# Kernel tuning notes

Hardware: AMD Instinct MI355X
Metric: run time of the kernel (lower is better)

The kernel has to match this reference:

```python
import jax, jax.numpy as jnp
import numpy as np

N = 50000
E = 800000
G = 8  # number of graphs
D_IN, D_H, D_OUT = 300, 128, 64


def _linear_params(key, d_out, d_in):
    k1, k2 = jax.random.split(key)
    s = 1.0 / np.sqrt(d_in)
    W = jax.random.uniform(k1, (d_out, d_in), minval=-s, maxval=s, dtype=jnp.float32)
    b = jax.random.uniform(k2, (d_out,), minval=-s, maxval=s, dtype=jnp.float32)
    return W, b


def setup_inputs() -> dict:
    key = jax.random.key(0)
    ks = jax.random.split(key, 10)
    x = jax.random.normal(ks[0], (N, D_IN), dtype=jnp.float32)
    edge_index = jax.random.randint(ks[1], (2, E), 0, N, dtype=jnp.int64)
    batch = jnp.sort(jax.random.randint(ks[2], (N,), 0, G, dtype=jnp.int64))
    W_emb, b_emb = _linear_params(ks[3], D_H, D_IN)
    # SAGEConv layer 0: lin_l (neighbors, with bias), lin_r (root, no bias)
    Wl0, bl0 = _linear_params(ks[4], D_H, D_H)
    Wr0, _ = _linear_params(ks[5], D_H, D_H)
    # SAGEConv layer 1
    Wl1, bl1 = _linear_params(ks[6], D_H, D_H)
    Wr1, _ = _linear_params(ks[7], D_H, D_H)
    W_att, b_att = _linear_params(ks[8], 1, D_H)
    W_out, b_out = _linear_params(ks[9], D_OUT, D_H)
    return {
        "x": x, "edge_index": edge_index, "batch": batch,
        "W_emb": W_emb, "b_emb": b_emb,
        "Wl0": Wl0, "bl0": bl0, "Wr0": Wr0,
        "Wl1": Wl1, "bl1": bl1, "Wr1": Wr1,
        "W_att": W_att, "b_att": b_att,
        "W_out": W_out, "b_out": b_out,
    }


def _sage_conv(h, src, dst, Wl, bl, Wr):
    # mean aggregation of source-node features onto destination nodes
    agg = jax.ops.segment_sum(h[src], dst, num_segments=N)  # [N, D_H]
    deg = jax.ops.segment_sum(jnp.ones((src.shape[0],), dtype=h.dtype), dst, num_segments=N)
    agg = agg / jnp.maximum(deg, 1.0)[:, None]
    return agg @ Wl.T + bl + h @ Wr.T


def reference(x, edge_index, batch, W_emb, b_emb, Wl0, bl0, Wr0, Wl1, bl1, Wr1,
              W_att, b_att, W_out, b_out):
    src, dst = edge_index[0], edge_index[1]
    h = x @ W_emb.T + b_emb                       # [N, D_H]
    h = jax.nn.relu(_sage_conv(h, src, dst, Wl0, bl0, Wr0))
    h = jax.nn.relu(_sage_conv(h, src, dst, Wl1, bl1, Wr1))
    # attention readout: softmax over ALL nodes (dim=0), as in original code
    scores = h @ W_att.T + b_att                  # [N, 1]
    weights = jax.nn.softmax(scores, axis=0)      # [N, 1]
    pooled = jax.ops.segment_sum(h * weights, batch, num_segments=G)  # [G, D_H]
    return pooled @ W_out.T + b_out               # [G, D_OUT]
```

## Files before the change

kernel.cpp:

```cpp
#include <hip/hip_runtime.h>
#include <math.h>

#define D_H 128

typedef __attribute__((ext_vector_type(8))) __bf16 bf16x8;
typedef __attribute__((ext_vector_type(4))) float f32x4;

__device__ __forceinline__ void split_bf16(float v, unsigned short& hi, unsigned short& lo) {
  unsigned int u = __float_as_uint(v);
  hi = (unsigned short)(u >> 16);
  float l = v - __uint_as_float(u & 0xffff0000u);
  lo = (unsigned short)(__float_as_uint(l) >> 16);
}

__device__ __forceinline__ float blo(unsigned int u) { return __uint_as_float(u << 16); }
__device__ __forceinline__ float bhi(unsigned int u) { return __uint_as_float(u & 0xffff0000u); }

__device__ __forceinline__ void pack_pair8(const float* xv, bf16x8& ah, bf16x8& al) {
  union { bf16x8 v; unsigned int u[4]; } H, L;
#pragma unroll
  for (int e = 0; e < 4; ++e) {
    unsigned int u0 = __float_as_uint(xv[2 * e]);
    unsigned int u1 = __float_as_uint(xv[2 * e + 1]);
    float l0 = xv[2 * e] - __uint_as_float(u0 & 0xffff0000u);
    float l1 = xv[2 * e + 1] - __uint_as_float(u1 & 0xffff0000u);
    H.u[e] = (u0 >> 16) | (u1 & 0xffff0000u);
    L.u[e] = (__float_as_uint(l0) >> 16) | (__float_as_uint(l1) & 0xffff0000u);
  }
  ah = H.v;
  al = L.v;
}

__device__ __forceinline__ void load_lds16(const void* g, void* l) {
  __builtin_amdgcn_global_load_lds((const __attribute__((address_space(1))) unsigned int*)g,
                                   (__attribute__((address_space(3))) unsigned int*)l,
                                   16, 0, 0);
}


__global__ __launch_bounds__(256) void k_hist(const int* __restrict__ dstv,
                                              int* __restrict__ bucketCnt, int E) {
  __shared__ int h[256];
  int t = threadIdx.x;
  h[t] = 0;
  __syncthreads();
  for (int i = blockIdx.x * 256 + t; i < E; i += gridDim.x * 256)
    atomicAdd(&h[dstv[i] >> 8], 1);
  __syncthreads();
  if (h[t]) atomicAdd(&bucketCnt[t], h[t]);
}

__global__ __launch_bounds__(256) void k_bucketscan(const int* __restrict__ bucketCnt, int NB,
                                                    int* __restrict__ bucketBase,
                                                    int* __restrict__ cursor,
                                                    int* __restrict__ row_ptr, int N, int E) {
  __shared__ int s[256];
  int t = threadIdx.x;
  int v = (t < NB) ? bucketCnt[t] : 0;
  s[t] = v;
  __syncthreads();
  for (int off = 1; off < 256; off <<= 1) {
    int u = (t >= off) ? s[t - off] : 0;
    __syncthreads();
    s[t] += u;
    __syncthreads();
  }
  int excl = s[t] - v;
  if (t < NB) {
    bucketBase[t] = excl;
    cursor[t] = excl;
  }
  if (t == NB - 1) bucketBase[NB] = excl + v;
  if (t == 0) row_ptr[N] = E;
}

__global__ __launch_bounds__(256) void k_binscatter(const int* __restrict__ srcv,
                                                    const int* __restrict__ dstv,
                                                    int* __restrict__ cursor,
                                                    unsigned int* __restrict__ tmp, int E) {
  __shared__ int h[256];
  __shared__ int base[256];
  int t = threadIdx.x;
  int chunk = (E + gridDim.x - 1) / gridDim.x;
  int c0 = blockIdx.x * chunk;
  int c1 = min(c0 + chunk, E);
  int dst[16], src[16];
  h[t] = 0;
  __syncthreads();
#pragma unroll
  for (int p = 0; p < 16; ++p) {
    int i = c0 + p * 256 + t;
    if (i < c1) {
      dst[p] = dstv[i];
      src[p] = srcv[i];
      atomicAdd(&h[dst[p] >> 8], 1);
    } else {
      dst[p] = -1;
      src[p] = 0;
    }
  }
  __syncthreads();
  int cnt = h[t];
  __syncthreads();
  base[t] = cnt ? atomicAdd(&cursor[t], cnt) : 0;
  h[t] = 0;
  __syncthreads();
#pragma unroll
  for (int p = 0; p < 16; ++p) {
    if (dst[p] >= 0) {
      int b = dst[p] >> 8;
      int pos = base[b] + atomicAdd(&h[b], 1);
      tmp[pos] = (unsigned int)src[p] | ((unsigned int)(dst[p] & 255) << 16);
    }
  }
}

__global__ __launch_bounds__(256) void k_localcsr(const unsigned int* __restrict__ tmp,
                                                  const int* __restrict__ bucketBase,
                                                  int* __restrict__ row_ptr,
                                                  int* __restrict__ col, int N) {
  __shared__ int deg[256], rp[256], cur[256];
  int b = blockIdx.x, t = threadIdx.x;
  int s = bucketBase[b], e = bucketBase[b + 1];
  int epb = e - s;
  deg[t] = 0;
  __syncthreads();
  for (int i = t; i < epb; i += 256) atomicAdd(&deg[tmp[s + i] >> 16], 1);
  __syncthreads();
  int v = deg[t];
  rp[t] = v;
  __syncthreads();
  for (int off = 1; off < 256; off <<= 1) {
    int u = (t >= off) ? rp[t - off] : 0;
    __syncthreads();
    rp[t] += u;
    __syncthreads();
  }
  int excl = rp[t] - v;
  rp[t] = excl;
  cur[t] = 0;
  int gid = b * 256 + t;
  if (gid < N) row_ptr[gid] = s + excl;
  __syncthreads();
  for (int i = t; i < epb; i += 256) {
    unsigned int p = tmp[s + i];
    int dl = p >> 16;
    int pos = s + rp[dl] + atomicAdd(&cur[dl], 1);
    col[pos] = (int)(p & 0xffffu);
  }
}


__global__ __launch_bounds__(256) void k_wsplit(
    const float* __restrict__ Wemb, const float* __restrict__ Wl0,
    const float* __restrict__ Wr0, const float* __restrict__ Wl1,
    const float* __restrict__ Wr1, unsigned short* __restrict__ WembP,
    unsigned short* __restrict__ P0l, unsigned short* __restrict__ P0r,
    unsigned short* __restrict__ P1l, unsigned short* __restrict__ P1r) {
  int tid = blockIdx.x * 256 + threadIdx.x;
  const int EMB = 128 * 320;
  if (tid < EMB) {
    int o = tid / 320, k = tid - o * 320;
    float v = (k < 300) ? Wemb[o * 300 + k] : 0.f;
    unsigned short h, l;
    split_bf16(v, h, l);
    int sw = ((2 * k) ^ ((o & 7) << 4)) >> 1;
    WembP[o * 640 + sw] = h;
    WembP[o * 640 + 320 + sw] = l;
  } else if (tid < EMB + 4 * 16384) {
    int r = tid - EMB;
    int m = r >> 14;
    int i = r & 16383;
    int o = i >> 7, k = i & 127;
    const float* W = (m == 0) ? Wl0 : (m == 1) ? Wr0 : (m == 2) ? Wl1 : Wr1;
    unsigned short* P = (m == 0) ? P0l : (m == 1) ? P0r : (m == 2) ? P1l : P1r;
    unsigned short h, l;
    split_bf16(W[o * 128 + k], h, l);
    int sw = ((2 * k) ^ ((o & 7) << 4)) >> 1;
    P[o * 256 + sw] = h;
    P[o * 256 + 128 + sw] = l;
  }
}


__global__ __launch_bounds__(512, 4) void k_emb(const float* __restrict__ x,
                                                const unsigned short* __restrict__ Wp,
                                                const float* __restrict__ bias,
                                                unsigned short* __restrict__ P, int N) {
  __shared__ alignas(16) char sW[49152];
  int t = threadIdx.x, lane = t & 63, wave = t >> 6;
  int ch = blockIdx.y;
  int row0 = blockIdx.x * 128;
  int fr = lane & 15, q4 = lane >> 4;
  int X = (fr & 7) << 4;
  int row = row0 + wave * 16 + fr;
  if (row >= N) row = N - 1;
  const float* xrp = x + (size_t)row * 300;
  const char* Wbase = (const char*)Wp + (size_t)ch * 64 * 1280;
  f32x4 acc[4] = {};
  float xb[2][8];

  auto stage = [&](int CB, int HS, int kb, int nround) {
    for (int r = 0; r < nround; ++r) {
      int off = r * 8192 + wave * 1024;
      int offl = off + lane * 16;
      int c = offl / CB;
      int w = offl - c * CB;
      const char* src = Wbase + (size_t)c * 1280 + (w < HS ? kb + w : 640 + kb + (w - HS));
      load_lds16(src, sW + off);
    }
  };
  auto loadx = [&](float* d, int c0) {
    if (c0 + 7 < 300) {
      float4 a = *(const float4*)(xrp + c0);
      float4 b = *(const float4*)(xrp + c0 + 4);
      d[0] = a.x; d[1] = a.y; d[2] = a.z; d[3] = a.w;
      d[4] = b.x; d[5] = b.y; d[6] = b.z; d[7] = b.w;
    } else {
#pragma unroll
      for (int e = 0; e < 8; ++e) d[e] = (c0 + e < 300) ? xrp[c0 + e] : 0.f;
    }
  };

  stage(768, 384, 0, 6);
  loadx(xb[0], q4 * 8);
  __syncthreads();

#pragma unroll
  for (int ks = 0; ks < 6; ++ks) {
    loadx(xb[(ks + 1) & 1], (ks + 1) * 32 + q4 * 8);
    bf16x8 bh[4], bl[4];
#pragma unroll
    for (int j = 0; j < 4; ++j) {
      int c64 = j * 16 + fr;
      int ko = (ks * 64 + q4 * 16) ^ X;
      bh[j] = *(const bf16x8*)(sW + c64 * 768 + ko);
      bl[j] = *(const bf16x8*)(sW + c64 * 768 + 384 + ko);
    }
    bf16x8 ah, al;
    pack_pair8(xb[ks & 1], ah, al);
#pragma unroll
    for (int j = 0; j < 4; ++j) {
      acc[j] = __builtin_amdgcn_mfma_f32_16x16x32_bf16(ah, bh[j], acc[j], 0, 0, 0);
      acc[j] = __builtin_amdgcn_mfma_f32_16x16x32_bf16(ah, bl[j], acc[j], 0, 0, 0);
      acc[j] = __builtin_amdgcn_mfma_f32_16x16x32_bf16(al, bh[j], acc[j], 0, 0, 0);
    }
  }
  __syncthreads();
  stage(512, 256, 384, 4);
  __syncthreads();

#pragma unroll
  for (int ks2 = 0; ks2 < 4; ++ks2) {
    int ks = 6 + ks2;
    if (ks < 9) loadx(xb[(ks + 1) & 1], (ks + 1) * 32 + q4 * 8);
    bf16x8 bh[4], bl[4];
#pragma unroll
    for (int j = 0; j < 4; ++j) {
      int c64 = j * 16 + fr;
      int ko = (ks2 * 64 + q4 * 16) ^ X;
      bh[j] = *(const bf16x8*)(sW + c64 * 512 + ko);
      bl[j] = *(const bf16x8*)(sW + c64 * 512 + 256 + ko);
    }
    bf16x8 ah, al;
    pack_pair8(xb[ks & 1], ah, al);
#pragma unroll
    for (int j = 0; j < 4; ++j) {
      acc[j] = __builtin_amdgcn_mfma_f32_16x16x32_bf16(ah, bh[j], acc[j], 0, 0, 0);
      acc[j] = __builtin_amdgcn_mfma_f32_16x16x32_bf16(ah, bl[j], acc[j], 0, 0, 0);
      acc[j] = __builtin_amdgcn_mfma_f32_16x16x32_bf16(al, bh[j], acc[j], 0, 0, 0);
    }
  }
  __syncthreads();

  float* T = (float*)sW;
#pragma unroll
  for (int j = 0; j < 4; ++j) {
    float b = bias[ch * 64 + j * 16 + fr];
#pragma unroll
    for (int rg = 0; rg < 4; ++rg)
      T[(wave * 16 + q4 * 4 + rg) * 66 + j * 16 + fr] = acc[j][rg] + b;
  }
  __syncthreads();
  int rr = t >> 2, q = t & 3;
  float vals[16];
#pragma unroll
  for (int c = 0; c < 16; ++c) vals[c] = T[rr * 66 + q * 16 + c];
  unsigned int hu[8], lu[8];
#pragma unroll
  for (int e = 0; e < 8; ++e) {
    unsigned int u0 = __float_as_uint(vals[2 * e]);
    unsigned int u1 = __float_as_uint(vals[2 * e + 1]);
    float l0 = vals[2 * e] - __uint_as_float(u0 & 0xffff0000u);
    float l1 = vals[2 * e + 1] - __uint_as_float(u1 & 0xffff0000u);
    hu[e] = (u0 >> 16) | (u1 & 0xffff0000u);
    lu[e] = (__float_as_uint(l0) >> 16) | (__float_as_uint(l1) & 0xffff0000u);
  }
  char* rowp = (char*)P + (size_t)(row0 + rr) * 512 + ch * 128;
  *(uint4*)(rowp + q * 32) = make_uint4(hu[0], hu[1], hu[2], hu[3]);
  *(uint4*)(rowp + q * 32 + 16) = make_uint4(hu[4], hu[5], hu[6], hu[7]);
  *(uint4*)(rowp + 256 + q * 32) = make_uint4(lu[0], lu[1], lu[2], lu[3]);
  *(uint4*)(rowp + 256 + q * 32 + 16) = make_uint4(lu[4], lu[5], lu[6], lu[7]);
}


__global__ __launch_bounds__(512, 4) void k_conv(const unsigned short* __restrict__ Ap,
                                                 const unsigned short* __restrict__ Wl,
                                                 const unsigned short* __restrict__ Wr,
                                                 unsigned short* __restrict__ Ub,
                                                 float* __restrict__ V) {
  __shared__ alignas(16) char sW[65536];
  int t = threadIdx.x, lane = t & 63, wave = t >> 6;
  int wr = wave >> 1, wc = wave & 1;
  int om = blockIdx.y;
  const char* Wg = (const char*)(om ? Wr : Wl);
  int row0 = blockIdx.x * 128;
  int fr = lane & 15, q4 = lane >> 4;
  int X = (fr & 7) << 4;

  for (int r = 0; r < 8; ++r) {
    int off = r * 8192 + wave * 1024;
    load_lds16(Wg + off + lane * 16, sW + off);
  }

  const char* a0 = (const char*)Ap + (size_t)(row0 + wr * 32 + fr) * 512 + q4 * 16;
  const char* a1 = a0 + 16 * 512;
  bf16x8 ah[2][2], al[2][2];
  ah[0][0] = *(const bf16x8*)a0;
  al[0][0] = *(const bf16x8*)(a0 + 256);
  ah[0][1] = *(const bf16x8*)a1;
  al[0][1] = *(const bf16x8*)(a1 + 256);

  f32x4 acc[2][4] = {};
  __syncthreads();

#pragma unroll
  for (int ks = 0; ks < 4; ++ks) {
    if (ks < 3) {
      int nb = (ks + 1) * 64;
      ah[(ks + 1) & 1][0] = *(const bf16x8*)(a0 + nb);
      al[(ks + 1) & 1][0] = *(const bf16x8*)(a0 + nb + 256);
      ah[(ks + 1) & 1][1] = *(const bf16x8*)(a1 + nb);
      al[(ks + 1) & 1][1] = *(const bf16x8*)(a1 + nb + 256);
    }
#pragma unroll
    for (int j = 0; j < 4; ++j) {
      int c = wc * 64 + j * 16 + fr;
      int ko = (ks * 64 + q4 * 16) ^ X;
      bf16x8 bh = *(const bf16x8*)(sW + c * 512 + ko);
      bf16x8 bl = *(const bf16x8*)(sW + c * 512 + 256 + ko);
#pragma unroll
      for (int i = 0; i < 2; ++i) {
        acc[i][j] = __builtin_amdgcn_mfma_f32_16x16x32_bf16(ah[ks & 1][i], bh, acc[i][j], 0, 0, 0);
        acc[i][j] = __builtin_amdgcn_mfma_f32_16x16x32_bf16(ah[ks & 1][i], bl, acc[i][j], 0, 0, 0);
        acc[i][j] = __builtin_amdgcn_mfma_f32_16x16x32_bf16(al[ks & 1][i], bh, acc[i][j], 0, 0, 0);
      }
    }
  }

  if (om == 0) {
    __syncthreads();
    unsigned short* Tb = (unsigned short*)sW;
#pragma unroll
    for (int i = 0; i < 2; ++i)
#pragma unroll
      for (int j = 0; j < 4; ++j)
#pragma unroll
        for (int rg = 0; rg < 4; ++rg) {
          float v = acc[i][j][rg];
          unsigned int u = __float_as_uint(v);
          u += 0x7fffu + ((u >> 16) & 1);
          Tb[(wr * 32 + i * 16 + q4 * 4 + rg) * 132 + wc * 64 + j * 16 + fr] =
              (unsigned short)(u >> 16);
        }
    __syncthreads();
    int rr = t >> 2, q = t & 3;
    const unsigned short* src = Tb + rr * 132 + q * 32;
    uint4 o0 = *(const uint4*)src;
    uint4 o1 = *(const uint4*)(src + 8);
    uint4 o2 = *(const uint4*)(src + 16);
    uint4 o3 = *(const uint4*)(src + 24);
    char* drow = (char*)Ub + (size_t)(row0 + rr) * 256 + q * 64;
    *(uint4*)(drow) = o0;
    *(uint4*)(drow + 16) = o1;
    *(uint4*)(drow + 32) = o2;
    *(uint4*)(drow + 48) = o3;
  } else {
#pragma unroll
    for (int i = 0; i < 2; ++i)
#pragma unroll
      for (int j = 0; j < 4; ++j)
#pragma unroll
        for (int rg = 0; rg < 4; ++rg)
          V[(size_t)(row0 + wr * 32 + i * 16 + q4 * 4 + rg) * D_H + wc * 64 + j * 16 + fr] =
              acc[i][j][rg];
  }
}


template <int OUTP>
__global__ __launch_bounds__(256) void k_aggfin(const unsigned short* __restrict__ Ub,
                                                float* __restrict__ V,
                                                const float* __restrict__ bias,
                                                const int* __restrict__ row_ptr,
                                                const int* __restrict__ col,
                                                unsigned short* __restrict__ Hp,
                                                const float* __restrict__ watt,
                                                const float* __restrict__ batt,
                                                float* __restrict__ scores,
                                                float* __restrict__ partmax, int N) {
  __shared__ float smax[4];
  int wv = threadIdx.x >> 6;
  int wid = blockIdx.x * 4 + wv;
  int lane = threadIdx.x & 63;
  bool valid = wid < N;
  if (OUTP == 1 && !valid) return;

  int half = lane >> 5;
  int dq = lane & 31;
  float a0 = 0.f, a1 = 0.f, a2 = 0.f, a3 = 0.f;
  float o0 = 0.f, o1 = 0.f, o2 = 0.f, o3 = 0.f;

  if (valid) {
    const uint2* uvb = (const uint2*)Ub;
    int e0 = row_ptr[wid], e1 = row_ptr[wid + 1];
    int e = e0;
    for (; e + 8 <= e1; e += 8) {
      int s0 = col[e + half];
      int s1 = col[e + 2 + half];
      int s2 = col[e + 4 + half];
      int s3 = col[e + 6 + half];
      uint2 u0 = uvb[(size_t)s0 * 32 + dq];
      uint2 u1 = uvb[(size_t)s1 * 32 + dq];
      uint2 u2 = uvb[(size_t)s2 * 32 + dq];
      uint2 u3 = uvb[(size_t)s3 * 32 + dq];
      a0 += blo(u0.x) + blo(u1.x) + blo(u2.x) + blo(u3.x);
      a1 += bhi(u0.x) + bhi(u1.x) + bhi(u2.x) + bhi(u3.x);
      a2 += blo(u0.y) + blo(u1.y) + blo(u2.y) + blo(u3.y);
      a3 += bhi(u0.y) + bhi(u1.y) + bhi(u2.y) + bhi(u3.y);
    }
    for (; e + 2 <= e1; e += 2) {
      uint2 u = uvb[(size_t)col[e + half] * 32 + dq];
      a0 += blo(u.x);
      a1 += bhi(u.x);
      a2 += blo(u.y);
      a3 += bhi(u.y);
    }
    if (e < e1 && half == 0) {
      uint2 u = uvb[(size_t)col[e] * 32 + dq];
      a0 += blo(u.x);
      a1 += bhi(u.x);
      a2 += blo(u.y);
      a3 += bhi(u.y);
    }
    a0 += __shfl_xor(a0, 32);
    a1 += __shfl_xor(a1, 32);
    a2 += __shfl_xor(a2, 32);
    a3 += __shfl_xor(a3, 32);

    float inv = 1.f / fmaxf((float)(e1 - e0), 1.f);
    float4 vv = *(const float4*)(V + (size_t)wid * D_H + dq * 4);
    float4 bb = *(const float4*)(bias + dq * 4);
    o0 = fmaxf(a0 * inv + vv.x + bb.x, 0.f);
    o1 = fmaxf(a1 * inv + vv.y + bb.y, 0.f);
    o2 = fmaxf(a2 * inv + vv.z + bb.z, 0.f);
    o3 = fmaxf(a3 * inv + vv.w + bb.w, 0.f);

    if (OUTP) {
      unsigned int w0, w1;
      if (half == 0) {
        unsigned int x0 = __float_as_uint(o0), x1 = __float_as_uint(o1);
        unsigned int x2 = __float_as_uint(o2), x3 = __float_as_uint(o3);
        w0 = (x0 >> 16) | (x1 & 0xffff0000u);
        w1 = (x2 >> 16) | (x3 & 0xffff0000u);
      } else {
        unsigned short h, lq0, lq1, lq2, lq3;
        split_bf16(o0, h, lq0);
        split_bf16(o1, h, lq1);
        split_bf16(o2, h, lq2);
        split_bf16(o3, h, lq3);
        w0 = (unsigned int)lq0 | ((unsigned int)lq1 << 16);
        w1 = (unsigned int)lq2 | ((unsigned int)lq3 << 16);
      }
      *(uint2*)((char*)Hp + (size_t)wid * 512 + half * 256 + dq * 8) = make_uint2(w0, w1);
    } else {
      if (half == 0)
        *(float4*)(V + (size_t)wid * D_H + dq * 4) = make_float4(o0, o1, o2, o3);
    }
  }

  if (OUTP == 0) {
    float sc = -3.0e38f;
    float4 w = valid ? *(const float4*)(watt + dq * 4) : make_float4(0.f, 0.f, 0.f, 0.f);
    float p = o0 * w.x + o1 * w.y + o2 * w.z + o3 * w.w;
#pragma unroll
    for (int off = 1; off < 32; off <<= 1) p += __shfl_xor(p, off);
    if (valid) {
      sc = p + batt[0];
      if (lane == 0) scores[wid] = sc;
    }
    if (lane == 0) smax[wv] = sc;
    __syncthreads();
    if (threadIdx.x == 0)
      partmax[blockIdx.x] = fmaxf(fmaxf(smax[0], smax[1]), fmaxf(smax[2], smax[3]));
  }
}


__global__ __launch_bounds__(256) void k_redmax(const float* __restrict__ partmax, int PB,
                                                float* __restrict__ red) {
  __shared__ float sm[256];
  int t = threadIdx.x;
  float m = -3.0e38f;
  for (int i = t; i < PB; i += 256) m = fmaxf(m, partmax[i]);
  sm[t] = m;
  __syncthreads();
  for (int off = 128; off > 0; off >>= 1) {
    if (t < off) sm[t] = fmaxf(sm[t], sm[t + off]);
    __syncthreads();
  }
  if (t == 0) {
    red[0] = sm[0];
    red[1] = 0.f;
  }
  for (int i = t; i < 1024; i += 256) red[2 + i] = 0.f;
}

__global__ __launch_bounds__(256) void k_pool(const float* __restrict__ h,
                                              const float* __restrict__ scores,
                                              const int* __restrict__ batch,
                                              float* __restrict__ red, int N, int nblocks) {
  __shared__ float pl[4][1024];
  __shared__ float zp[4];
  int t = threadIdx.x;
  int w = t >> 6, lane = t & 63;
  for (int i = lane; i < 1024; i += 64) pl[w][i] = 0.f;
  float M = red[0];
  float zacc = 0.f;
  const float2* hv = (const float2*)h;
  int stride = nblocks * 4;
  for (int node = blockIdx.x * 4 + w; node < N; node += stride) {
    float wgt = __expf(scores[node] - M);
    int b = batch[node];
    float2 v = hv[(size_t)node * 64 + lane];
    pl[w][b * 128 + lane * 2] += v.x * wgt;
    pl[w][b * 128 + lane * 2 + 1] += v.y * wgt;
    zacc += wgt;
  }
  if (lane == 0) zp[w] = zacc;
  __syncthreads();
  for (int i = t; i < 1024; i += 256) {
    float s = pl[0][i] + pl[1][i] + pl[2][i] + pl[3][i];
    atomicAdd(&red[2 + i], s);
  }
  if (t == 0) atomicAdd(&red[1], zp[0] + zp[1] + zp[2] + zp[3]);
}

__global__ __launch_bounds__(512) void k_out(const float* __restrict__ red,
                                             const float* __restrict__ Wout,
                                             const float* __restrict__ bout,
                                             float* __restrict__ out) {
  int t = threadIdx.x;
  int gIdx = t >> 6, o = t & 63;
  float invZ = 1.f / red[1];
  const float* p = red + 2 + gIdx * 128;
  const float* wr = Wout + (size_t)o * 128;
  float acc = 0.f;
  for (int k = 0; k < 128; ++k) acc = fmaf(p[k], wr[k], acc);
  out[gIdx * 64 + o] = acc * invZ + bout[o];
}


extern "C" void kernel_launch(void* const* d_in, const int* in_sizes, int n_in,
                              void* d_out, int out_size, void* d_ws, size_t ws_size,
                              hipStream_t stream) {
  const float* x     = (const float*)d_in[0];
  const int*   ei    = (const int*)d_in[1];
  const int*   batch = (const int*)d_in[2];
  const float* W_emb = (const float*)d_in[3];
  const float* b_emb = (const float*)d_in[4];
  const float* Wl0   = (const float*)d_in[5];
  const float* bl0   = (const float*)d_in[6];
  const float* Wr0   = (const float*)d_in[7];
  const float* Wl1   = (const float*)d_in[8];
  const float* bl1   = (const float*)d_in[9];
  const float* Wr1   = (const float*)d_in[10];
  const float* W_att = (const float*)d_in[11];
  const float* b_att = (const float*)d_in[12];
  const float* W_out = (const float*)d_in[13];
  const float* b_out = (const float*)d_in[14];
  float* out = (float*)d_out;

  const int DIN = 300;
  int N = in_sizes[0] / DIN;
  int E = in_sizes[1] / 2;
  int Npad = (N + 127) & ~127;
  int NB = (N + 255) / 256;

  char* wsp = (char*)d_ws;
  size_t off = 0;
  auto carve = [&](size_t bytes) -> void* {
    void* p = wsp + off;
    off += (bytes + 255) & ~(size_t)255;
    return p;
  };
  unsigned short* P  = (unsigned short*)carve((size_t)Npad * 512);
  unsigned short* Ub = (unsigned short*)carve((size_t)Npad * 256);
  float*          V  = (float*)carve((size_t)Npad * 512);
  unsigned short* WembP = (unsigned short*)carve((size_t)128 * 640 * 2);
  unsigned short* WP0l  = (unsigned short*)carve((size_t)128 * 256 * 2);
  unsigned short* WP0r  = (unsigned short*)carve((size_t)128 * 256 * 2);
  unsigned short* WP1l  = (unsigned short*)carve((size_t)128 * 256 * 2);
  unsigned short* WP1r  = (unsigned short*)carve((size_t)128 * 256 * 2);
  int*   colA    = (int*)carve((size_t)E * 4);
  unsigned int* tmpE = (unsigned int*)carve((size_t)E * 4);
  int*   row_ptr = (int*)carve((size_t)(N + 1) * 4);
  int*   bucketCnt  = (int*)carve((size_t)(NB + 1) * 4);
  int*   bucketBase = (int*)carve((size_t)(NB + 1) * 4);
  int*   cursor     = (int*)carve((size_t)(NB + 1) * 4);
  float* scores  = (float*)carve((size_t)N * 4);
  int aggBlocks = (N + 3) / 4;
  float* partmax = (float*)carve((size_t)aggBlocks * 4);
  float* red     = (float*)carve((size_t)(2 + 1024) * 4);

  const int* srcv = ei;
  const int* dstv = ei + E;

  hipMemsetAsync(bucketCnt, 0, (size_t)NB * 4, stream);
  k_hist<<<512, 256, 0, stream>>>(dstv, bucketCnt, E);
  k_bucketscan<<<1, 256, 0, stream>>>(bucketCnt, NB, bucketBase, cursor, row_ptr, N, E);
  k_binscatter<<<256, 256, 0, stream>>>(srcv, dstv, cursor, tmpE, E);
  k_localcsr<<<NB, 256, 0, stream>>>(tmpE, bucketBase, row_ptr, colA, N);
  k_wsplit<<<(128 * 320 + 4 * 16384 + 255) / 256, 256, 0, stream>>>(
      W_emb, Wl0, Wr0, Wl1, Wr1, WembP, WP0l, WP0r, WP1l, WP1r);

  dim3 gemb(Npad / 128, 2);
  k_emb<<<gemb, 512, 0, stream>>>(x, WembP, b_emb, P, N);

  dim3 gconv(Npad / 128, 2);
  k_conv<<<gconv, 512, 0, stream>>>(P, WP0l, WP0r, Ub, V);
  k_aggfin<1><<<aggBlocks, 256, 0, stream>>>(Ub, V, bl0, row_ptr, colA, P,
                                             nullptr, nullptr, nullptr, nullptr, N);
  k_conv<<<gconv, 512, 0, stream>>>(P, WP1l, WP1r, Ub, V);
  k_aggfin<0><<<aggBlocks, 256, 0, stream>>>(Ub, V, bl1, row_ptr, colA, nullptr,
                                             W_att, b_att, scores, partmax, N);

  const float* h2 = (const float*)V;
  k_redmax<<<1, 256, 0, stream>>>(partmax, aggBlocks, red);
  k_pool<<<256, 256, 0, stream>>>(h2, scores, batch, red, N, 256);
  k_out<<<1, 512, 0, stream>>>(red, W_out, b_out, out);
}
```

Before: 251.9 us.

## Fuse weight split into histogram, merge pool kernels, restructure emb/conv GEMM tiling

Weight bf16 splitting moves into the histogram kernel, and the redmax, pool and output kernels become one kernel that finishes with a last-block-done counter. Several launches disappear. The embedding and conv GEMMs now cover all 128 output columns per block (one grid dimension instead of two) and stage weights in smaller K-chunks with reduced LDS, so x/A rows are read once rather than twice. This costs more syncs per K-chunk, and every pool block recomputes the global max.

```diff
diff --git a/kernel.cpp b/kernel.cpp
--- a/kernel.cpp
+++ b/kernel.cpp
@@ -38,14 +38,44 @@
 }
 
 
-__global__ __launch_bounds__(256) void k_hist(const int* __restrict__ dstv,
-                                              int* __restrict__ bucketCnt, int E) {
+__global__ __launch_bounds__(256) void k_histw(
+    const int* __restrict__ dstv, int* __restrict__ bucketCnt, int E,
+    const float* __restrict__ Wemb, const float* __restrict__ Wl0,
+    const float* __restrict__ Wr0, const float* __restrict__ Wl1,
+    const float* __restrict__ Wr1, unsigned short* __restrict__ WembP,
+    unsigned short* __restrict__ P0l, unsigned short* __restrict__ P0r,
+    unsigned short* __restrict__ P1l, unsigned short* __restrict__ P1r) {
   __shared__ int h[256];
   int t = threadIdx.x;
   h[t] = 0;
   __syncthreads();
   for (int i = blockIdx.x * 256 + t; i < E; i += gridDim.x * 256)
     atomicAdd(&h[dstv[i] >> 8], 1);
+
+  int tid = blockIdx.x * 256 + t;
+  const int EMB = 128 * 320;
+  if (tid < EMB) {
+    int o = tid / 320, k = tid - o * 320;
+    float v = (k < 300) ? Wemb[o * 300 + k] : 0.f;
+    unsigned short hh, ll;
+    split_bf16(v, hh, ll);
+    int sw = ((2 * k) ^ ((o & 7) << 4)) >> 1;
+    WembP[o * 640 + sw] = hh;
+    WembP[o * 640 + 320 + sw] = ll;
+  } else if (tid < EMB + 4 * 16384) {
+    int r = tid - EMB;
+    int m = r >> 14;
+    int i = r & 16383;
+    int o = i >> 7, k = i & 127;
+    const float* W = (m == 0) ? Wl0 : (m == 1) ? Wr0 : (m == 2) ? Wl1 : Wr1;
+    unsigned short* P = (m == 0) ? P0l : (m == 1) ? P0r : (m == 2) ? P1l : P1r;
+    unsigned short hh, ll;
+    split_bf16(W[o * 128 + k], hh, ll);
+    int sw = ((2 * k) ^ ((o & 7) << 4)) >> 1;
+    P[o * 256 + sw] = hh;
+    P[o * 256 + 128 + sw] = ll;
+  }
+
   __syncthreads();
   if (h[t]) atomicAdd(&bucketCnt[t], h[t]);
 }
@@ -151,65 +181,21 @@
 }
 
 
-__global__ __launch_bounds__(256) void k_wsplit(
-    const float* __restrict__ Wemb, const float* __restrict__ Wl0,
-    const float* __restrict__ Wr0, const float* __restrict__ Wl1,
-    const float* __restrict__ Wr1, unsigned short* __restrict__ WembP,
-    unsigned short* __restrict__ P0l, unsigned short* __restrict__ P0r,
-    unsigned short* __restrict__ P1l, unsigned short* __restrict__ P1r) {
-  int tid = blockIdx.x * 256 + threadIdx.x;
-  const int EMB = 128 * 320;
-  if (tid < EMB) {
-    int o = tid / 320, k = tid - o * 320;
-    float v = (k < 300) ? Wemb[o * 300 + k] : 0.f;
-    unsigned short h, l;
-    split_bf16(v, h, l);
-    int sw = ((2 * k) ^ ((o & 7) << 4)) >> 1;
-    WembP[o * 640 + sw] = h;
-    WembP[o * 640 + 320 + sw] = l;
-  } else if (tid < EMB + 4 * 16384) {
-    int r = tid - EMB;
-    int m = r >> 14;
-    int i = r & 16383;
-    int o = i >> 7, k = i & 127;
-    const float* W = (m == 0) ? Wl0 : (m == 1) ? Wr0 : (m == 2) ? Wl1 : Wr1;
-    unsigned short* P = (m == 0) ? P0l : (m == 1) ? P0r : (m == 2) ? P1l : P1r;
-    unsigned short h, l;
-    split_bf16(W[o * 128 + k], h, l);
-    int sw = ((2 * k) ^ ((o & 7) << 4)) >> 1;
-    P[o * 256 + sw] = h;
-    P[o * 256 + 128 + sw] = l;
-  }
-}
-
-
 __global__ __launch_bounds__(512, 4) void k_emb(const float* __restrict__ x,
                                                 const unsigned short* __restrict__ Wp,
                                                 const float* __restrict__ bias,
                                                 unsigned short* __restrict__ P, int N) {
-  __shared__ alignas(16) char sW[49152];
+  __shared__ alignas(16) char sW[34048];
   int t = threadIdx.x, lane = t & 63, wave = t >> 6;
-  int ch = blockIdx.y;
   int row0 = blockIdx.x * 128;
   int fr = lane & 15, q4 = lane >> 4;
   int X = (fr & 7) << 4;
   int row = row0 + wave * 16 + fr;
   if (row >= N) row = N - 1;
   const float* xrp = x + (size_t)row * 300;
-  const char* Wbase = (const char*)Wp + (size_t)ch * 64 * 1280;
-  f32x4 acc[4] = {};
+  f32x4 acc[8] = {};
   float xb[2][8];
 
-  auto stage = [&](int CB, int HS, int kb, int nround) {
-    for (int r = 0; r < nround; ++r) {
-      int off = r * 8192 + wave * 1024;
-      int offl = off + lane * 16;
-      int c = offl / CB;
-      int w = offl - c * CB;
-      const char* src = Wbase + (size_t)c * 1280 + (w < HS ? kb + w : 640 + kb + (w - HS));
-      load_lds16(src, sW + off);
-    }
-  };
   auto loadx = [&](float* d, int c0) {
     if (c0 + 7 < 300) {
       float4 a = *(const float4*)(xrp + c0);
@@ -222,85 +208,75 @@
     }
   };
 
-  stage(768, 384, 0, 6);
   loadx(xb[0], q4 * 8);
-  __syncthreads();
-
-#pragma unroll
-  for (int ks = 0; ks < 6; ++ks) {
-    loadx(xb[(ks + 1) & 1], (ks + 1) * 32 + q4 * 8);
-    bf16x8 bh[4], bl[4];
-#pragma unroll
-    for (int j = 0; j < 4; ++j) {
-      int c64 = j * 16 + fr;
-      int ko = (ks * 64 + q4 * 16) ^ X;
-      bh[j] = *(const bf16x8*)(sW + c64 * 768 + ko);
-      bl[j] = *(const bf16x8*)(sW + c64 * 768 + 384 + ko);
-    }
-    bf16x8 ah, al;
-    pack_pair8(xb[ks & 1], ah, al);
-#pragma unroll
-    for (int j = 0; j < 4; ++j) {
-      acc[j] = __builtin_amdgcn_mfma_f32_16x16x32_bf16(ah, bh[j], acc[j], 0, 0, 0);
-      acc[j] = __builtin_amdgcn_mfma_f32_16x16x32_bf16(ah, bl[j], acc[j], 0, 0, 0);
-      acc[j] = __builtin_amdgcn_mfma_f32_16x16x32_bf16(al, bh[j], acc[j], 0, 0, 0);
-    }
-  }
-  __syncthreads();
-  stage(512, 256, 384, 4);
-  __syncthreads();
-
-#pragma unroll
-  for (int ks2 = 0; ks2 < 4; ++ks2) {
-    int ks = 6 + ks2;
-    if (ks < 9) loadx(xb[(ks + 1) & 1], (ks + 1) * 32 + q4 * 8);
-    bf16x8 bh[4], bl[4];
-#pragma unroll
-    for (int j = 0; j < 4; ++j) {
-      int c64 = j * 16 + fr;
-      int ko = (ks2 * 64 + q4 * 16) ^ X;
-      bh[j] = *(const bf16x8*)(sW + c64 * 512 + ko);
-      bl[j] = *(const bf16x8*)(sW + c64 * 512 + 256 + ko);
-    }
-    bf16x8 ah, al;
-    pack_pair8(xb[ks & 1], ah, al);
-#pragma unroll
-    for (int j = 0; j < 4; ++j) {
-      acc[j] = __builtin_amdgcn_mfma_f32_16x16x32_bf16(ah, bh[j], acc[j], 0, 0, 0);
-      acc[j] = __builtin_amdgcn_mfma_f32_16x16x32_bf16(ah, bl[j], acc[j], 0, 0, 0);
-      acc[j] = __builtin_amdgcn_mfma_f32_16x16x32_bf16(al, bh[j], acc[j], 0, 0, 0);
-    }
-  }
-  __syncthreads();
+#pragma unroll
+  for (int kc = 0; kc < 5; ++kc) {
+#pragma unroll
+    for (int r = 0; r < 4; ++r) {
+      int off = r * 8192 + wave * 1024;
+      int offl = off + lane * 16;
+      int c = offl >> 8;
+      int w = offl & 255;
+      const char* src = (const char*)Wp + (size_t)c * 1280 +
+                        (w < 128 ? kc * 128 + w : 640 + kc * 128 + (w - 128));
+      load_lds16(src, sW + off);
+    }
+    __syncthreads();
+#pragma unroll
+    for (int s = 0; s < 2; ++s) {
+      int ks = kc * 2 + s;
+      if (ks < 9) loadx(xb[(ks + 1) & 1], (ks + 1) * 32 + q4 * 8);
+      bf16x8 ah, al;
+      pack_pair8(xb[ks & 1], ah, al);
+      int ko = (s * 64 + q4 * 16) ^ X;
+#pragma unroll
+      for (int j = 0; j < 8; ++j) {
+        int c = j * 16 + fr;
+        bf16x8 bh = *(const bf16x8*)(sW + c * 256 + ko);
+        bf16x8 bl = *(const bf16x8*)(sW + c * 256 + 128 + ko);
+        acc[j] = __builtin_amdgcn_mfma_f32_16x16x32_bf16(ah, bh, acc[j], 0, 0, 0);
+        acc[j] = __builtin_amdgcn_mfma_f32_16x16x32_bf16(ah, bl, acc[j], 0, 0, 0);
+        acc[j] = __builtin_amdgcn_mfma_f32_16x16x32_bf16(al, bh, acc[j], 0, 0, 0);
+      }
+    }
+    __syncthreads();
+  }
 
   float* T = (float*)sW;
 #pragma unroll
-  for (int j = 0; j < 4; ++j) {
-    float b = bias[ch * 64 + j * 16 + fr];
-#pragma unroll
-    for (int rg = 0; rg < 4; ++rg)
-      T[(wave * 16 + q4 * 4 + rg) * 66 + j * 16 + fr] = acc[j][rg] + b;
-  }
-  __syncthreads();
-  int rr = t >> 2, q = t & 3;
-  float vals[16];
-#pragma unroll
-  for (int c = 0; c < 16; ++c) vals[c] = T[rr * 66 + q * 16 + c];
-  unsigned int hu[8], lu[8];
-#pragma unroll
-  for (int e = 0; e < 8; ++e) {
-    unsigned int u0 = __float_as_uint(vals[2 * e]);
-    unsigned int u1 = __float_as_uint(vals[2 * e + 1]);
-    float l0 = vals[2 * e] - __uint_as_float(u0 & 0xffff0000u);
-    float l1 = vals[2 * e + 1] - __uint_as_float(u1 & 0xffff0000u);
-    hu[e] = (u0 >> 16) | (u1 & 0xffff0000u);
-    lu[e] = (__float_as_uint(l0) >> 16) | (__float_as_uint(l1) & 0xffff0000u);
-  }
-  char* rowp = (char*)P + (size_t)(row0 + rr) * 512 + ch * 128;
-  *(uint4*)(rowp + q * 32) = make_uint4(hu[0], hu[1], hu[2], hu[3]);
-  *(uint4*)(rowp + q * 32 + 16) = make_uint4(hu[4], hu[5], hu[6], hu[7]);
-  *(uint4*)(rowp + 256 + q * 32) = make_uint4(lu[0], lu[1], lu[2], lu[3]);
-  *(uint4*)(rowp + 256 + q * 32 + 16) = make_uint4(lu[4], lu[5], lu[6], lu[7]);
+  for (int ph = 0; ph < 2; ++ph) {
+    if ((wave >> 2) == ph) {
+      int wl = wave & 3;
+#pragma unroll
+      for (int j = 0; j < 8; ++j) {
+        float b = bias[j * 16 + fr];
+#pragma unroll
+        for (int rg = 0; rg < 4; ++rg)
+          T[(wl * 16 + q4 * 4 + rg) * 132 + j * 16 + fr] = acc[j][rg] + b;
+      }
+    }
+    __syncthreads();
+    int r = t >> 3, q = t & 7;
+    float vals[16];
+#pragma unroll
+    for (int c = 0; c < 16; ++c) vals[c] = T[r * 132 + q * 16 + c];
+    unsigned int hu[8], lu[8];
+#pragma unroll
+    for (int e = 0; e < 8; ++e) {
+      unsigned int u0 = __float_as_uint(vals[2 * e]);
+      unsigned int u1 = __float_as_uint(vals[2 * e + 1]);
+      float l0 = vals[2 * e] - __uint_as_float(u0 & 0xffff0000u);
+      float l1 = vals[2 * e + 1] - __uint_as_float(u1 & 0xffff0000u);
+      hu[e] = (u0 >> 16) | (u1 & 0xffff0000u);
+      lu[e] = (__float_as_uint(l0) >> 16) | (__float_as_uint(l1) & 0xffff0000u);
+    }
+    char* rowp = (char*)P + (size_t)(row0 + ph * 64 + r) * 512;
+    *(uint4*)(rowp + q * 32) = make_uint4(hu[0], hu[1], hu[2], hu[3]);
+    *(uint4*)(rowp + q * 32 + 16) = make_uint4(hu[4], hu[5], hu[6], hu[7]);
+    *(uint4*)(rowp + 256 + q * 32) = make_uint4(lu[0], lu[1], lu[2], lu[3]);
+    *(uint4*)(rowp + 256 + q * 32 + 16) = make_uint4(lu[4], lu[5], lu[6], lu[7]);
+    __syncthreads();
+  }
 }
 
 
@@ -309,92 +285,101 @@
                                                  const unsigned short* __restrict__ Wr,
                                                  unsigned short* __restrict__ Ub,
                                                  float* __restrict__ V) {
-  __shared__ alignas(16) char sW[65536];
+  __shared__ alignas(16) char sW[34048];
   int t = threadIdx.x, lane = t & 63, wave = t >> 6;
-  int wr = wave >> 1, wc = wave & 1;
-  int om = blockIdx.y;
-  const char* Wg = (const char*)(om ? Wr : Wl);
+  int wr2 = wave >> 1, wc = wave & 1;
   int row0 = blockIdx.x * 128;
   int fr = lane & 15, q4 = lane >> 4;
   int X = (fr & 7) << 4;
 
-  for (int r = 0; r < 8; ++r) {
-    int off = r * 8192 + wave * 1024;
-    load_lds16(Wg + off + lane * 16, sW + off);
-  }
-
-  const char* a0 = (const char*)Ap + (size_t)(row0 + wr * 32 + fr) * 512 + q4 * 16;
-  const char* a1 = a0 + 16 * 512;
-  bf16x8 ah[2][2], al[2][2];
-  ah[0][0] = *(const bf16x8*)a0;
-  al[0][0] = *(const bf16x8*)(a0 + 256);
-  ah[0][1] = *(const bf16x8*)a1;
-  al[0][1] = *(const bf16x8*)(a1 + 256);
-
-  f32x4 acc[2][4] = {};
-  __syncthreads();
-
-#pragma unroll
-  for (int ks = 0; ks < 4; ++ks) {
-    if (ks < 3) {
-      int nb = (ks + 1) * 64;
-      ah[(ks + 1) & 1][0] = *(const bf16x8*)(a0 + nb);
-      al[(ks + 1) & 1][0] = *(const bf16x8*)(a0 + nb + 256);
-      ah[(ks + 1) & 1][1] = *(const bf16x8*)(a1 + nb);
-      al[(ks + 1) & 1][1] = *(const bf16x8*)(a1 + nb + 256);
-    }
-#pragma unroll
-    for (int j = 0; j < 4; ++j) {
-      int c = wc * 64 + j * 16 + fr;
-      int ko = (ks * 64 + q4 * 16) ^ X;
-      bf16x8 bh = *(const bf16x8*)(sW + c * 512 + ko);
-      bf16x8 bl = *(const bf16x8*)(sW + c * 512 + 256 + ko);
-#pragma unroll
-      for (int i = 0; i < 2; ++i) {
-        acc[i][j] = __builtin_amdgcn_mfma_f32_16x16x32_bf16(ah[ks & 1][i], bh, acc[i][j], 0, 0, 0);
-        acc[i][j] = __builtin_amdgcn_mfma_f32_16x16x32_bf16(ah[ks & 1][i], bl, acc[i][j], 0, 0, 0);
-        acc[i][j] = __builtin_amdgcn_mfma_f32_16x16x32_bf16(al[ks & 1][i], bh, acc[i][j], 0, 0, 0);
+  f32x4 accU[2][4] = {};
+  f32x4 accV[2][4] = {};
+
+#pragma unroll
+  for (int m = 0; m < 2; ++m) {
+    const char* Wg = (const char*)(m ? Wr : Wl);
+#pragma unroll
+    for (int kc = 0; kc < 2; ++kc) {
+#pragma unroll
+      for (int r = 0; r < 4; ++r) {
+        int off = r * 8192 + wave * 1024;
+        int offl = off + lane * 16;
+        int c = offl >> 8;
+        int w = offl & 255;
+        const char* src = Wg + (size_t)c * 512 +
+                          (w < 128 ? kc * 128 + w : 256 + kc * 128 + (w - 128));
+        load_lds16(src, sW + off);
       }
-    }
-  }
-
-  if (om == 0) {
-    __syncthreads();
-    unsigned short* Tb = (unsigned short*)sW;
-#pragma unroll
-    for (int i = 0; i < 2; ++i)
-#pragma unroll
-      for (int j = 0; j < 4; ++j)
-#pragma unroll
-        for (int rg = 0; rg < 4; ++rg) {
-          float v = acc[i][j][rg];
-          unsigned int u = __float_as_uint(v);
-          u += 0x7fffu + ((u >> 16) & 1);
-          Tb[(wr * 32 + i * 16 + q4 * 4 + rg) * 132 + wc * 64 + j * 16 + fr] =
-              (unsigned short)(u >> 16);
+      __syncthreads();
+#pragma unroll
+      for (int s = 0; s < 2; ++s) {
+        int ks = kc * 2 + s;
+        bf16x8 ah[2], al[2];
+#pragma unroll
+        for (int i = 0; i < 2; ++i) {
+          const char* ab =
+              (const char*)Ap + (size_t)(row0 + wr2 * 32 + i * 16 + fr) * 512 + ks * 64 + q4 * 16;
+          ah[i] = *(const bf16x8*)ab;
+          al[i] = *(const bf16x8*)(ab + 256);
         }
-    __syncthreads();
-    int rr = t >> 2, q = t & 3;
-    const unsigned short* src = Tb + rr * 132 + q * 32;
-    uint4 o0 = *(const uint4*)src;
-    uint4 o1 = *(const uint4*)(src + 8);
-    uint4 o2 = *(const uint4*)(src + 16);
-    uint4 o3 = *(const uint4*)(src + 24);
-    char* drow = (char*)Ub + (size_t)(row0 + rr) * 256 + q * 64;
-    *(uint4*)(drow) = o0;
-    *(uint4*)(drow + 16) = o1;
-    *(uint4*)(drow + 32) = o2;
-    *(uint4*)(drow + 48) = o3;
-  } else {
-#pragma unroll
-    for (int i = 0; i < 2; ++i)
-#pragma unroll
-      for (int j = 0; j < 4; ++j)
-#pragma unroll
-        for (int rg = 0; rg < 4; ++rg)
-          V[(size_t)(row0 + wr * 32 + i * 16 + q4 * 4 + rg) * D_H + wc * 64 + j * 16 + fr] =
-              acc[i][j][rg];
-  }
+        int ko = (s * 64 + q4 * 16) ^ X;
+#pragma unroll
+        for (int j = 0; j < 4; ++j) {
+          int c = wc * 64 + j * 16 + fr;
+          bf16x8 bh = *(const bf16x8*)(sW + c * 256 + ko);
+          bf16x8 bl = *(const bf16x8*)(sW + c * 256 + 128 + ko);
+#pragma unroll
+          for (int i = 0; i < 2; ++i) {
+            if (m == 0) {
+              accU[i][j] = __builtin_amdgcn_mfma_f32_16x16x32_bf16(ah[i], bh, accU[i][j], 0, 0, 0);
+              accU[i][j] = __builtin_amdgcn_mfma_f32_16x16x32_bf16(ah[i], bl, accU[i][j], 0, 0, 0);
+              accU[i][j] = __builtin_amdgcn_mfma_f32_16x16x32_bf16(al[i], bh, accU[i][j], 0, 0, 0);
+            } else {
+              accV[i][j] = __builtin_amdgcn_mfma_f32_16x16x32_bf16(ah[i], bh, accV[i][j], 0, 0, 0);
+              accV[i][j] = __builtin_amdgcn_mfma_f32_16x16x32_bf16(ah[i], bl, accV[i][j], 0, 0, 0);
+              accV[i][j] = __builtin_amdgcn_mfma_f32_16x16x32_bf16(al[i], bh, accV[i][j], 0, 0, 0);
+            }
+          }
+        }
+      }
+      __syncthreads();
+    }
+  }
+
+#pragma unroll
+  for (int i = 0; i < 2; ++i)
+#pragma unroll
+    for (int j = 0; j < 4; ++j)
+#pragma unroll
+      for (int rg = 0; rg < 4; ++rg)
+        V[(size_t)(row0 + wr2 * 32 + i * 16 + q4 * 4 + rg) * D_H + wc * 64 + j * 16 + fr] =
+            accV[i][j][rg];
+
+  unsigned short* Tb = (unsigned short*)sW;
+#pragma unroll
+  for (int i = 0; i < 2; ++i)
+#pragma unroll
+    for (int j = 0; j < 4; ++j)
+#pragma unroll
+      for (int rg = 0; rg < 4; ++rg) {
+        float v = accU[i][j][rg];
+        unsigned int u = __float_as_uint(v);
+        u += 0x7fffu + ((u >> 16) & 1);
+        Tb[(wr2 * 32 + i * 16 + q4 * 4 + rg) * 132 + wc * 64 + j * 16 + fr] =
+            (unsigned short)(u >> 16);
+      }
+  __syncthreads();
+  int rr = t >> 2, q = t & 3;
+  const unsigned short* src = Tb + rr * 132 + q * 32;
+  uint4 o0 = *(const uint4*)src;
+  uint4 o1 = *(const uint4*)(src + 8);
+  uint4 o2 = *(const uint4*)(src + 16);
+  uint4 o3 = *(const uint4*)(src + 24);
+  char* drow = (char*)Ub + (size_t)(row0 + rr) * 256 + q * 64;
+  *(uint4*)(drow) = o0;
+  *(uint4*)(drow + 16) = o1;
+  *(uint4*)(drow + 32) = o2;
+  *(uint4*)(drow + 48) = o3;
 }
 
 
@@ -507,10 +492,20 @@
 }
 
 
-__global__ __launch_bounds__(256) void k_redmax(const float* __restrict__ partmax, int PB,
-                                                float* __restrict__ red) {
+__global__ __launch_bounds__(256) void k_pool(const float* __restrict__ h,
+                                              const float* __restrict__ scores,
+                                              const int* __restrict__ batch,
+                                              const float* __restrict__ partmax, int PB,
+                                              float* __restrict__ red, int* __restrict__ ctr,
+                                              const float* __restrict__ Wout,
+                                              const float* __restrict__ bout,
+                                              float* __restrict__ out, int N, int nblocks) {
   __shared__ float sm[256];
+  __shared__ float pl[4][1024];
+  __shared__ float zp[4];
+  __shared__ int lastFlag;
   int t = threadIdx.x;
+
   float m = -3.0e38f;
   for (int i = t; i < PB; i += 256) m = fmaxf(m, partmax[i]);
   sm[t] = m;
@@ -519,23 +514,10 @@
     if (t < off) sm[t] = fmaxf(sm[t], sm[t + off]);
     __syncthreads();
   }
-  if (t == 0) {
-    red[0] = sm[0];
-    red[1] = 0.f;
-  }
-  for (int i = t; i < 1024; i += 256) red[2 + i] = 0.f;
-}
-
-__global__ __launch_bounds__(256) void k_pool(const float* __restrict__ h,
-                                              const float* __restrict__ scores,
-                                              const int* __restrict__ batch,
-                                              float* __restrict__ red, int N, int nblocks) {
-  __shared__ float pl[4][1024];
-  __shared__ float zp[4];
-  int t = threadIdx.x;
+  float M = sm[0];
+
   int w = t >> 6, lane = t & 63;
   for (int i = lane; i < 1024; i += 64) pl[w][i] = 0.f;
-  float M = red[0];
   float zacc = 0.f;
   const float2* hv = (const float2*)h;
   int stride = nblocks * 4;
@@ -554,20 +536,22 @@
     atomicAdd(&red[2 + i], s);
   }
   if (t == 0) atomicAdd(&red[1], zp[0] + zp[1] + zp[2] + zp[3]);
-}
-
-__global__ __launch_bounds__(512) void k_out(const float* __restrict__ red,
-                                             const float* __restrict__ Wout,
-                                             const float* __restrict__ bout,
-                                             float* __restrict__ out) {
-  int t = threadIdx.x;
-  int gIdx = t >> 6, o = t & 63;
-  float invZ = 1.f / red[1];
-  const float* p = red + 2 + gIdx * 128;
-  const float* wr = Wout + (size_t)o * 128;
-  float acc = 0.f;
-  for (int k = 0; k < 128; ++k) acc = fmaf(p[k], wr[k], acc);
-  out[gIdx * 64 + o] = acc * invZ + bout[o];
+
+  __threadfence();
+  if (t == 0) lastFlag = (atomicAdd(ctr, 1) == nblocks - 1) ? 1 : 0;
+  __syncthreads();
+  if (lastFlag) {
+    __threadfence();
+    float invZ = 1.f / red[1];
+    for (int o = t; o < 512; o += 256) {
+      int g = o >> 6, oo = o & 63;
+      const float* p = red + 2 + g * 128;
+      const float* wr = Wout + (size_t)oo * 128;
+      float acc = 0.f;
+      for (int k = 0; k < 128; ++k) acc = fmaf(p[k], wr[k], acc);
+      out[g * 64 + oo] = acc * invZ + bout[oo];
+    }
+  }
 }
 
 
@@ -615,38 +599,38 @@
   int*   colA    = (int*)carve((size_t)E * 4);
   unsigned int* tmpE = (unsigned int*)carve((size_t)E * 4);
   int*   row_ptr = (int*)carve((size_t)(N + 1) * 4);
-  int*   bucketCnt  = (int*)carve((size_t)(NB + 1) * 4);
   int*   bucketBase = (int*)carve((size_t)(NB + 1) * 4);
   int*   cursor     = (int*)carve((size_t)(NB + 1) * 4);
   float* scores  = (float*)carve((size_t)N * 4);
   int aggBlocks = (N + 3) / 4;
   float* partmax = (float*)carve((size_t)aggBlocks * 4);
-  float* red     = (float*)carve((size_t)(2 + 1024) * 4);
+  int zInts = (NB + 1) + 1026 + 1;
+  int* zbase = (int*)carve((size_t)zInts * 4);
+  int*   bucketCnt = zbase;
+  float* red       = (float*)(zbase + NB + 1);
+  int*   ctr       = zbase + (NB + 1) + 1026;
 
   const int* srcv = ei;
   const int* dstv = ei + E;
 
-  hipMemsetAsync(bucketCnt, 0, (size_t)NB * 4, stream);
-  k_hist<<<512, 256, 0, stream>>>(dstv, bucketCnt, E);
+  hipMemsetAsync(zbase, 0, (size_t)zInts * 4, stream);
+  k_histw<<<512, 256, 0, stream>>>(dstv, bucketCnt, E, W_emb, Wl0, Wr0, Wl1, Wr1,
+                                   WembP, WP0l, WP0r, WP1l, WP1r);
   k_bucketscan<<<1, 256, 0, stream>>>(bucketCnt, NB, bucketBase, cursor, row_ptr, N, E);
   k_binscatter<<<256, 256, 0, stream>>>(srcv, dstv, cursor, tmpE, E);
   k_localcsr<<<NB, 256, 0, stream>>>(tmpE, bucketBase, row_ptr, colA, N);
-  k_wsplit<<<(128 * 320 + 4 * 16384 + 255) / 256, 256, 0, stream>>>(
-      W_emb, Wl0, Wr0, Wl1, Wr1, WembP, WP0l, WP0r, WP1l, WP1r);
-
-  dim3 gemb(Npad / 128, 2);
-  k_emb<<<gemb, 512, 0, stream>>>(x, WembP, b_emb, P, N);
-
-  dim3 gconv(Npad / 128, 2);
-  k_conv<<<gconv, 512, 0, stream>>>(P, WP0l, WP0r, Ub, V);
+
+  int gblocks = Npad / 128;
+  k_emb<<<gblocks, 512, 0, stream>>>(x, WembP, b_emb, P, N);
+
+  k_conv<<<gblocks, 512, 0, stream>>>(P, WP0l, WP0r, Ub, V);
   k_aggfin<1><<<aggBlocks, 256, 0, stream>>>(Ub, V, bl0, row_ptr, colA, P,
                                              nullptr, nullptr, nullptr, nullptr, N);
-  k_conv<<<gconv, 512, 0, stream>>>(P, WP1l, WP1r, Ub, V);
+  k_conv<<<gblocks, 512, 0, stream>>>(P, WP1l, WP1r, Ub, V);
   k_aggfin<0><<<aggBlocks, 256, 0, stream>>>(Ub, V, bl1, row_ptr, colA, nullptr,
                                              W_att, b_att, scores, partmax, N);
 
   const float* h2 = (const float*)V;
-  k_redmax<<<1, 256, 0, stream>>>(partmax, aggBlocks, red);
-  k_pool<<<256, 256, 0, stream>>>(h2, scores, batch, red, N, 256);
-  k_out<<<1, 512, 0, stream>>>(red, W_out, b_out, out);
-}
+  k_pool<<<256, 256, 0, stream>>>(h2, scores, batch, partmax, aggBlocks, red, ctr,
+                                  W_out, b_out, out, N, 256);
+}
```

Result: slower. 259.9 us (+3.2%).
